# Kernel tuning notes

Hardware: AMD Instinct MI355X
Metric: run time of the kernel (lower is better)

## Reference

```python
import jax, jax.numpy as jnp
import numpy as np

N_EDGES = 1_600_000
N_NODES = 100_000
D_FEAT = 64


def setup_inputs() -> dict:
    key = jax.random.key(0)
    k1, k2 = jax.random.split(key)
    messages = jax.random.normal(k1, (N_EDGES, D_FEAT), dtype=jnp.float32)
    dst = jax.random.randint(k2, (N_EDGES,), 0, N_NODES, dtype=jnp.int64)
    return {"messages": messages, "dst": dst, "num_nodes": N_NODES}


def reference(messages, dst, num_nodes):
    # aggregators = ['sum', 'mean', 'max', 'std'] (module default)
    N = num_nodes
    ones = jnp.ones((dst.shape[0],), dtype=messages.dtype)
    # sum aggregation
    s = jax.ops.segment_sum(messages, dst, num_segments=N)  # [N, D]
    # degree, clamped to >= 1 (as in scatter_count)
    deg = jnp.maximum(jax.ops.segment_sum(ones, dst, num_segments=N), 1.0)[:, None]  # [N, 1]
    # mean aggregation
    mean = s / deg
    # max aggregation; empty segments yield -inf -> replaced with 0
    mx = jax.ops.segment_max(messages, dst, num_segments=N)
    mx = jnp.where(jnp.isfinite(mx), mx, jnp.zeros((), dtype=messages.dtype))
    # std aggregation: mean of squared deviations from per-node mean
    sq_diff = (messages - mean[dst]) ** 2
    var = jax.ops.segment_sum(sq_diff, dst, num_segments=N) / deg
    std = jnp.sqrt(var + 1e-8)
    return jnp.concatenate([s, mean, mx, std], axis=-1)  # [N, 4*D]
```

## Files before the change

### kernel.cpp

```cpp
#include <hip/hip_runtime.h>
#include <float.h>


__global__ void zero_counts(int* __restrict__ counts, int N) {
    int i = blockIdx.x * 256 + threadIdx.x;
    if (i < N) counts[i] = 0;
}

__global__ void hist(const int* __restrict__ dst, int stride, int* __restrict__ counts, int E) {
    int e = blockIdx.x * 256 + threadIdx.x;
    if (e < E) {
        int n = (stride == 2) ? (int)((const long long*)dst)[e] : dst[e];
        atomicAdd(&counts[n], 1);
    }
}

__global__ void scan1(const int* __restrict__ counts, int* __restrict__ offsets,
                      int* __restrict__ partials, int N) {
    __shared__ int s[256];
    int t = threadIdx.x;
    int i = blockIdx.x * 256 + t;
    int x = (i < N) ? counts[i] : 0;
    s[t] = x;
    __syncthreads();
    for (int o = 1; o < 256; o <<= 1) {
        int y = (t >= o) ? s[t - o] : 0;
        __syncthreads();
        s[t] += y;
        __syncthreads();
    }
    if (i < N) offsets[i] = s[t] - x;
    if (t == 255) partials[blockIdx.x] = s[255];
}

__global__ void scan2(int* __restrict__ partials, int NB) {
    __shared__ int s[512];
    int t = threadIdx.x;
    int x = (t < NB) ? partials[t] : 0;
    s[t] = x;
    __syncthreads();
    for (int o = 1; o < 512; o <<= 1) {
        int y = (t >= o) ? s[t - o] : 0;
        __syncthreads();
        s[t] += y;
        __syncthreads();
    }
    if (t < NB) partials[t] = s[t] - x;
}

__global__ void scan3(int* __restrict__ offsets, const int* __restrict__ partials,
                      int* __restrict__ cursor, int N, int E) {
    int i = blockIdx.x * 256 + threadIdx.x;
    if (i < N) {
        int off = offsets[i] + partials[blockIdx.x];
        offsets[i] = off;
        cursor[i] = off;
    }
    if (i == 0) offsets[N] = E;
}

__global__ void permscatter(const int* __restrict__ dst, int stride,
                            int* __restrict__ cursor, int* __restrict__ perm, int E) {
    int e = blockIdx.x * 256 + threadIdx.x;
    if (e < E) {
        int n = (stride == 2) ? (int)((const long long*)dst)[e] : dst[e];
        int pos = atomicAdd(&cursor[n], 1);
        perm[pos] = e;
    }
}

__global__ void reduce(const float* __restrict__ msg, const int* __restrict__ perm,
                       const int* __restrict__ offsets, float* __restrict__ out, int N) {
    int node = blockIdx.x * 4 + (threadIdx.x >> 6);
    if (node >= N) return;
    int lane = threadIdx.x & 63;
    int beg = offsets[node];
    int end = offsets[node + 1];

    float s0 = 0.f, s1 = 0.f, s2 = 0.f, s3 = 0.f;
    float q0 = 0.f, q1 = 0.f, q2 = 0.f, q3 = 0.f;
    float m0 = -FLT_MAX, m1 = -FLT_MAX, m2 = -FLT_MAX, m3 = -FLT_MAX;

    const float* mp = msg + lane;

    for (int base = beg; base < end; base += 64) {
        int cnt = end - base;
        if (cnt > 64) cnt = 64;
        int idx = base + lane;
        if (idx >= end) idx = end - 1;
        int eid_l = perm[idx];

        int j = 0;
        for (; j + 4 <= cnt; j += 4) {
            int e0 = __shfl(eid_l, j + 0);
            int e1 = __shfl(eid_l, j + 1);
            int e2 = __shfl(eid_l, j + 2);
            int e3 = __shfl(eid_l, j + 3);
            float v0 = mp[(long long)e0 << 6];
            float v1 = mp[(long long)e1 << 6];
            float v2 = mp[(long long)e2 << 6];
            float v3 = mp[(long long)e3 << 6];
            s0 += v0; q0 += v0 * v0; m0 = fmaxf(m0, v0);
            s1 += v1; q1 += v1 * v1; m1 = fmaxf(m1, v1);
            s2 += v2; q2 += v2 * v2; m2 = fmaxf(m2, v2);
            s3 += v3; q3 += v3 * v3; m3 = fmaxf(m3, v3);
        }
        for (; j < cnt; ++j) {
            int e = __shfl(eid_l, j);
            float v = mp[(long long)e << 6];
            s0 += v; q0 += v * v; m0 = fmaxf(m0, v);
        }
    }

    float s  = (s0 + s1) + (s2 + s3);
    float sq = (q0 + q1) + (q2 + q3);
    float mx = fmaxf(fmaxf(m0, m1), fmaxf(m2, m3));

    float deg  = fmaxf((float)(end - beg), 1.0f);
    float mean = s / deg;
    float var  = fmaxf(sq / deg - mean * mean, 0.0f);
    float mxo  = (end > beg) ? mx : 0.0f;

    float* base_out = out + (long long)node * 256;
    base_out[lane]       = s;
    base_out[64 + lane]  = mean;
    base_out[128 + lane] = mxo;
    base_out[192 + lane] = sqrtf(var + 1e-8f);
}

extern "C" void kernel_launch(void* const* d_in, const int* in_sizes, int n_in,
                              void* d_out, int out_size, void* d_ws, size_t ws_size,
                              hipStream_t stream) {
    const float* msg = (const float*)d_in[0];
    const int*   dst = (const int*)d_in[1];
    float* out = (float*)d_out;

    int E = in_sizes[0] / 64;
    int N = out_size / 256;
    int stride = (in_sizes[1] == 2 * E) ? 2 : 1;

    int* counts   = (int*)d_ws;
    int* offsets  = counts + N;
    int* cursor   = offsets + N + 1;
    int* partials = cursor + N;
    int* perm     = partials + 512;

    int NB_N = (N + 255) / 256;
    int NB_E = (E + 255) / 256;

    zero_counts<<<NB_N, 256, 0, stream>>>(counts, N);
    hist<<<NB_E, 256, 0, stream>>>(dst, stride, counts, E);
    scan1<<<NB_N, 256, 0, stream>>>(counts, offsets, partials, N);
    scan2<<<1, 512, 0, stream>>>(partials, NB_N);
    scan3<<<NB_N, 256, 0, stream>>>(offsets, partials, cursor, N, E);
    permscatter<<<NB_E, 256, 0, stream>>>(dst, stride, cursor, perm, E);
    reduce<<<(N + 3) / 4, 256, 0, stream>>>(msg, perm, offsets, out, N);
}
```

Baseline: 764.6 us.

## Fuse counting-sort preprocessing kernels into one cooperative kernel with grid syncs

Replaces the zero/histogram/three-stage scan/permutation-scatter launches with a single cooperative kernel that separates phases with grid-wide synchronisation. Index reads of the int64 destination array are vectorised as int4 pairs. The aim is to remove per-launch overhead and gaps between the small kernels. The cost is grid-sync latency and a fixed grid of 1024 blocks, which may reduce atomic parallelism; the old launches remain as a fallback if the cooperative launch fails.

Result: slower. 1.536 ms (+100.9%).

```diff
diff --git a/kernel.cpp b/kernel.cpp
--- a/kernel.cpp
+++ b/kernel.cpp
@@ -1,5 +1,120 @@
 #include <hip/hip_runtime.h>
+#include <hip/hip_cooperative_groups.h>
 #include <float.h>
+
+namespace cg = cooperative_groups;
+
+
+#define COOP_BLOCKS 1024
+#define BLK 256
+
+__global__ void __launch_bounds__(256, 4) fused_sort(
+    const int* __restrict__ dst, int stride,
+    int* __restrict__ counts, int* __restrict__ offsets, int* __restrict__ cursor,
+    int* __restrict__ partials, int* __restrict__ perm,
+    int N, int E, int NB_N)
+{
+    cg::grid_group grid = cg::this_grid();
+    const int tid = blockIdx.x * BLK + threadIdx.x;
+    const int nthreads = gridDim.x * BLK;
+
+    for (int i = tid; i < N; i += nthreads) counts[i] = 0;
+    __threadfence();
+    grid.sync();
+
+    if (stride == 2) {
+        const int4* d4 = (const int4*)dst;
+        int npair = E >> 1;
+        for (int p = tid; p < npair; p += nthreads) {
+            int4 v = d4[p];
+            atomicAdd(&counts[v.x], 1);
+            atomicAdd(&counts[v.z], 1);
+        }
+        for (int e = (npair << 1) + tid; e < E; e += nthreads)
+            atomicAdd(&counts[(int)((const long long*)dst)[e]], 1);
+    } else {
+        for (int e = tid; e < E; e += nthreads)
+            atomicAdd(&counts[dst[e]], 1);
+    }
+    __threadfence();
+    grid.sync();
+
+    {
+        int c = blockIdx.x;
+        if (c < NB_N) {
+            __shared__ int s[BLK];
+            int t = threadIdx.x;
+            int i = c * BLK + t;
+            int x = (i < N) ? counts[i] : 0;
+            s[t] = x;
+            __syncthreads();
+            for (int o = 1; o < BLK; o <<= 1) {
+                int y = (t >= o) ? s[t - o] : 0;
+                __syncthreads();
+                s[t] += y;
+                __syncthreads();
+            }
+            if (i < N) offsets[i] = s[t] - x;
+            if (t == BLK - 1) partials[c] = s[t];
+        }
+    }
+    __threadfence();
+    grid.sync();
+
+    if (blockIdx.x == 0) {
+        __shared__ int a[BLK];
+        int t = threadIdx.x;
+        int i0 = 2 * t, i1 = 2 * t + 1;
+        int x0 = (i0 < NB_N) ? partials[i0] : 0;
+        int x1 = (i1 < NB_N) ? partials[i1] : 0;
+        a[t] = x0 + x1;
+        __syncthreads();
+        for (int o = 1; o < BLK; o <<= 1) {
+            int y = (t >= o) ? a[t - o] : 0;
+            __syncthreads();
+            a[t] += y;
+            __syncthreads();
+        }
+        int excl = a[t] - (x0 + x1);
+        if (i0 < NB_N) partials[i0] = excl;
+        if (i1 < NB_N) partials[i1] = excl + x0;
+    }
+    __threadfence();
+    grid.sync();
+
+    for (int i = tid; i < N; i += nthreads) {
+        int off = offsets[i] + partials[i >> 8];
+        offsets[i] = off;
+        cursor[i] = off;
+    }
+    if (tid == 0) offsets[N] = E;
+    __threadfence();
+    grid.sync();
+
+    if (stride == 2) {
+        const int4* d4 = (const int4*)dst;
+        int npair = E >> 1;
+        for (int p = tid; p < npair; p += nthreads) {
+            int4 v = d4[p];
+            int e0 = 2 * p, e1 = 2 * p + 1;
+            int p0 = atomicAdd(&cursor[v.x], 1);
+            perm[p0] = e0;
+            int p1 = atomicAdd(&cursor[v.z], 1);
+            perm[p1] = e1;
+        }
+        for (int e = (npair << 1) + tid; e < E; e += nthreads) {
+            int n = (int)((const long long*)dst)[e];
+            int pos = atomicAdd(&cursor[n], 1);
+            perm[pos] = e;
+        }
+    } else {
+        for (int e = tid; e < E; e += nthreads) {
+            int n = dst[e];
+            int pos = atomicAdd(&cursor[n], 1);
+            perm[pos] = e;
+        }
+    }
+}
 
 
 __global__ void zero_counts(int* __restrict__ counts, int N) {
@@ -148,11 +263,26 @@
     int NB_N = (N + 255) / 256;
     int NB_E = (E + 255) / 256;
 
-    zero_counts<<<NB_N, 256, 0, stream>>>(counts, N);
-    hist<<<NB_E, 256, 0, stream>>>(dst, stride, counts, E);
-    scan1<<<NB_N, 256, 0, stream>>>(counts, offsets, partials, N);
-    scan2<<<1, 512, 0, stream>>>(partials, NB_N);
-    scan3<<<NB_N, 256, 0, stream>>>(offsets, partials, cursor, N, E);
-    permscatter<<<NB_E, 256, 0, stream>>>(dst, stride, cursor, perm, E);
+    {
+        const int* dst_a = dst; int stride_a = stride;
+        int* counts_a = counts; int* offsets_a = offsets; int* cursor_a = cursor;
+        int* partials_a = partials; int* perm_a = perm;
+        int N_a = N, E_a = E, NB_a = NB_N;
+        void* args[] = { (void*)&dst_a, (void*)&stride_a, (void*)&counts_a,
+                         (void*)&offsets_a, (void*)&cursor_a, (void*)&partials_a,
+                         (void*)&perm_a, (void*)&N_a, (void*)&E_a, (void*)&NB_a };
+        hipError_t err = hipLaunchCooperativeKernel((const void*)fused_sort,
+                                                    dim3(COOP_BLOCKS), dim3(BLK),
+                                                    args, 0, stream);
+        if (err != hipSuccess) {
+            zero_counts<<<NB_N, 256, 0, stream>>>(counts, N);
+            hist<<<NB_E, 256, 0, stream>>>(dst, stride, counts, E);
+            scan1<<<NB_N, 256, 0, stream>>>(counts, offsets, partials, N);
+            scan2<<<1, 512, 0, stream>>>(partials, NB_N);
+            scan3<<<NB_N, 256, 0, stream>>>(offsets, partials, cursor, N, E);
+            permscatter<<<NB_E, 256, 0, stream>>>(dst, stride, cursor, perm, E);
+        }
+    }
+
     reduce<<<(N + 3) / 4, 256, 0, stream>>>(msg, perm, offsets, out, N);
 }
```

## Record atomic ranks in histogram to drop second atomic pass and scan3

Applied to the files above, without the earlier changes.

The histogram kernel now keeps the atomicAdd return value as each edge's rank within its node. A non-atomic scatter then places each edge at local offset plus block partial plus rank, which removes the cursor-based atomic scatter and the scan3 fixup kernel. The reduce kernel computes segment begin and degree from the local offsets, partials and counts, and its edge loop gains an 8-way unrolled path. This costs an extra E-sized rank buffer in workspace, so the old path is kept as a fallback when the workspace is too small.

Measured after the change: 664.3 us. -13.1%, faster.

```diff
diff --git a/kernel.cpp b/kernel.cpp
--- a/kernel.cpp
+++ b/kernel.cpp
@@ -2,35 +2,48 @@
 #include <float.h>
 
 
+#define BLK 256
+
 __global__ void zero_counts(int* __restrict__ counts, int N) {
-    int i = blockIdx.x * 256 + threadIdx.x;
+    int i = blockIdx.x * BLK + threadIdx.x;
     if (i < N) counts[i] = 0;
 }
 
-__global__ void hist(const int* __restrict__ dst, int stride, int* __restrict__ counts, int E) {
-    int e = blockIdx.x * 256 + threadIdx.x;
-    if (e < E) {
-        int n = (stride == 2) ? (int)((const long long*)dst)[e] : dst[e];
-        atomicAdd(&counts[n], 1);
-    }
-}
-
-__global__ void scan1(const int* __restrict__ counts, int* __restrict__ offsets,
+__global__ void hist_rank(const int* __restrict__ dst, int stride,
+                          int* __restrict__ counts, int* __restrict__ rank, int E) {
+    int e = blockIdx.x * BLK + threadIdx.x;
+    if (e < E) {
+        int n = (stride == 2) ? (int)((const long long*)dst)[e] : dst[e];
+        rank[e] = atomicAdd(&counts[n], 1);
+    }
+}
+
+__global__ void scatter_rank(const int* __restrict__ dst, int stride,
+                             const int* __restrict__ lofs, const int* __restrict__ partials,
+                             const int* __restrict__ rank, int* __restrict__ perm, int E) {
+    int e = blockIdx.x * BLK + threadIdx.x;
+    if (e < E) {
+        int n = (stride == 2) ? (int)((const long long*)dst)[e] : dst[e];
+        perm[lofs[n] + partials[n >> 8] + rank[e]] = e;
+    }
+}
+
+__global__ void scan1(const int* __restrict__ counts, int* __restrict__ lofs,
                       int* __restrict__ partials, int N) {
-    __shared__ int s[256];
+    __shared__ int s[BLK];
     int t = threadIdx.x;
-    int i = blockIdx.x * 256 + t;
+    int i = blockIdx.x * BLK + t;
     int x = (i < N) ? counts[i] : 0;
     s[t] = x;
     __syncthreads();
-    for (int o = 1; o < 256; o <<= 1) {
+    for (int o = 1; o < BLK; o <<= 1) {
         int y = (t >= o) ? s[t - o] : 0;
         __syncthreads();
         s[t] += y;
         __syncthreads();
     }
-    if (i < N) offsets[i] = s[t] - x;
-    if (t == 255) partials[blockIdx.x] = s[255];
+    if (i < N) lofs[i] = s[t] - x;
+    if (t == BLK - 1) partials[blockIdx.x] = s[t];
 }
 
 __global__ void scan2(int* __restrict__ partials, int NB) {
@@ -48,20 +61,23 @@
     if (t < NB) partials[t] = s[t] - x;
 }
 
-__global__ void scan3(int* __restrict__ offsets, const int* __restrict__ partials,
-                      int* __restrict__ cursor, int N, int E) {
-    int i = blockIdx.x * 256 + threadIdx.x;
-    if (i < N) {
-        int off = offsets[i] + partials[blockIdx.x];
-        offsets[i] = off;
-        cursor[i] = off;
-    }
-    if (i == 0) offsets[N] = E;
+__global__ void hist(const int* __restrict__ dst, int stride, int* __restrict__ counts, int E) {
+    int e = blockIdx.x * BLK + threadIdx.x;
+    if (e < E) {
+        int n = (stride == 2) ? (int)((const long long*)dst)[e] : dst[e];
+        atomicAdd(&counts[n], 1);
+    }
+}
+
+__global__ void cursor_init(const int* __restrict__ lofs, const int* __restrict__ partials,
+                            int* __restrict__ cursor, int N) {
+    int i = blockIdx.x * BLK + threadIdx.x;
+    if (i < N) cursor[i] = lofs[i] + partials[i >> 8];
 }
 
 __global__ void permscatter(const int* __restrict__ dst, int stride,
                             int* __restrict__ cursor, int* __restrict__ perm, int E) {
-    int e = blockIdx.x * 256 + threadIdx.x;
+    int e = blockIdx.x * BLK + threadIdx.x;
     if (e < E) {
         int n = (stride == 2) ? (int)((const long long*)dst)[e] : dst[e];
         int pos = atomicAdd(&cursor[n], 1);
@@ -70,12 +86,14 @@
 }
 
 __global__ void reduce(const float* __restrict__ msg, const int* __restrict__ perm,
-                       const int* __restrict__ offsets, float* __restrict__ out, int N) {
+                       const int* __restrict__ lofs, const int* __restrict__ partials,
+                       const int* __restrict__ counts, float* __restrict__ out, int N) {
     int node = blockIdx.x * 4 + (threadIdx.x >> 6);
     if (node >= N) return;
     int lane = threadIdx.x & 63;
-    int beg = offsets[node];
-    int end = offsets[node + 1];
+    int beg = lofs[node] + partials[node >> 8];
+    int deg_i = counts[node];
+    int end = beg + deg_i;
 
     float s0 = 0.f, s1 = 0.f, s2 = 0.f, s3 = 0.f;
     float q0 = 0.f, q1 = 0.f, q2 = 0.f, q3 = 0.f;
@@ -91,6 +109,32 @@
         int eid_l = perm[idx];
 
         int j = 0;
+        for (; j + 8 <= cnt; j += 8) {
+            int e0 = __shfl(eid_l, j + 0);
+            int e1 = __shfl(eid_l, j + 1);
+            int e2 = __shfl(eid_l, j + 2);
+            int e3 = __shfl(eid_l, j + 3);
+            int e4 = __shfl(eid_l, j + 4);
+            int e5 = __shfl(eid_l, j + 5);
+            int e6 = __shfl(eid_l, j + 6);
+            int e7 = __shfl(eid_l, j + 7);
+            float v0 = mp[(long long)e0 << 6];
+            float v1 = mp[(long long)e1 << 6];
+            float v2 = mp[(long long)e2 << 6];
+            float v3 = mp[(long long)e3 << 6];
+            float v4 = mp[(long long)e4 << 6];
+            float v5 = mp[(long long)e5 << 6];
+            float v6 = mp[(long long)e6 << 6];
+            float v7 = mp[(long long)e7 << 6];
+            s0 += v0; q0 += v0 * v0; m0 = fmaxf(m0, v0);
+            s1 += v1; q1 += v1 * v1; m1 = fmaxf(m1, v1);
+            s2 += v2; q2 += v2 * v2; m2 = fmaxf(m2, v2);
+            s3 += v3; q3 += v3 * v3; m3 = fmaxf(m3, v3);
+            s0 += v4; q0 += v4 * v4; m0 = fmaxf(m0, v4);
+            s1 += v5; q1 += v5 * v5; m1 = fmaxf(m1, v5);
+            s2 += v6; q2 += v6 * v6; m2 = fmaxf(m2, v6);
+            s3 += v7; q3 += v7 * v7; m3 = fmaxf(m3, v7);
+        }
         for (; j + 4 <= cnt; j += 4) {
             int e0 = __shfl(eid_l, j + 0);
             int e1 = __shfl(eid_l, j + 1);
@@ -116,10 +160,10 @@
     float sq = (q0 + q1) + (q2 + q3);
     float mx = fmaxf(fmaxf(m0, m1), fmaxf(m2, m3));
 
-    float deg  = fmaxf((float)(end - beg), 1.0f);
+    float deg  = fmaxf((float)deg_i, 1.0f);
     float mean = s / deg;
     float var  = fmaxf(sq / deg - mean * mean, 0.0f);
-    float mxo  = (end > beg) ? mx : 0.0f;
+    float mxo  = (deg_i > 0) ? mx : 0.0f;
 
     float* base_out = out + (long long)node * 256;
     base_out[lane]       = s;
@@ -140,19 +184,32 @@
     int stride = (in_sizes[1] == 2 * E) ? 2 : 1;
 
     int* counts   = (int*)d_ws;
-    int* offsets  = counts + N;
-    int* cursor   = offsets + N + 1;
-    int* partials = cursor + N;
+    int* lofs     = counts + N;
+    int* partials = lofs + N;
     int* perm     = partials + 512;
-
-    int NB_N = (N + 255) / 256;
-    int NB_E = (E + 255) / 256;
-
-    zero_counts<<<NB_N, 256, 0, stream>>>(counts, N);
-    hist<<<NB_E, 256, 0, stream>>>(dst, stride, counts, E);
-    scan1<<<NB_N, 256, 0, stream>>>(counts, offsets, partials, N);
-    scan2<<<1, 512, 0, stream>>>(partials, NB_N);
-    scan3<<<NB_N, 256, 0, stream>>>(offsets, partials, cursor, N, E);
-    permscatter<<<NB_E, 256, 0, stream>>>(dst, stride, cursor, perm, E);
-    reduce<<<(N + 3) / 4, 256, 0, stream>>>(msg, perm, offsets, out, N);
-}
+    int* extra    = perm + E;
+
+    int NB_N = (N + BLK - 1) / BLK;
+    int NB_E = (E + BLK - 1) / BLK;
+
+    size_t need_rank = ((size_t)2 * N + 512 + (size_t)2 * E) * sizeof(int);
+
+    zero_counts<<<NB_N, BLK, 0, stream>>>(counts, N);
+
+    if (ws_size >= need_rank) {
+        int* rank = extra;
+        hist_rank<<<NB_E, BLK, 0, stream>>>(dst, stride, counts, rank, E);
+        scan1<<<NB_N, BLK, 0, stream>>>(counts, lofs, partials, N);
+        scan2<<<1, 512, 0, stream>>>(partials, NB_N);
+        scatter_rank<<<NB_E, BLK, 0, stream>>>(dst, stride, lofs, partials, rank, perm, E);
+    } else {
+        int* cursor = extra;
+        hist<<<NB_E, BLK, 0, stream>>>(dst, stride, counts, E);
+        scan1<<<NB_N, BLK, 0, stream>>>(counts, lofs, partials, N);
+        scan2<<<1, 512, 0, stream>>>(partials, NB_N);
+        cursor_init<<<NB_N, BLK, 0, stream>>>(lofs, partials, cursor, N);
+        permscatter<<<NB_E, BLK, 0, stream>>>(dst, stride, cursor, perm, E);
+    }
+
+    reduce<<<(N + 3) / 4, BLK, 0, stream>>>(msg, perm, lofs, partials, counts, out, N);
+}
```
